# Performance work log

Measured on AMD Instinct MI355X. Metric: run time of the kernel, lower is better.

Reference implementation:

```python
import jax, jax.numpy as jnp
import numpy as np

IN_C = 16
OUT_C = 16
GRID = 8
K = 3  # spline order
RANGE = (-1.0, 1.0)
COEF_M = GRID + K                       # number of B-spline coefficients per (in,out)
SIZE = IN_C * OUT_C * COEF_M + 2 * IN_C * OUT_C  # 3328: coef + univariate_w + residual_w


def _grid():
    # extended knot grid: grid_size intervals over RANGE, padded by K on each side
    h = (RANGE[1] - RANGE[0]) / GRID
    return (np.arange(-K, GRID + K + 1) * h + RANGE[0]).astype(np.float32)


def b_splines(x, grid):
    # x: (N, in) -> bases: (N, in, GRID + K) via Cox-de Boor recursion
    xg = x[..., None]
    bases = ((xg >= grid[:-1]) & (xg < grid[1:])).astype(x.dtype)
    for p in range(1, K + 1):
        left = (xg - grid[:-(p + 1)]) / (grid[p:-1] - grid[:-(p + 1)])
        right = (grid[p + 1:] - xg) / (grid[p + 1:] - grid[1:-p])
        bases = left * bases[..., :-1] + right * bases[..., 1:]
    return bases


def setup_inputs() -> dict:
    key = jax.random.key(0)
    k1, k2 = jax.random.split(key)
    x = jax.random.normal(k1, (2, IN_C, 128, 128), jnp.float32)
    w = jax.random.normal(k2, (2, SIZE, 128, 128), jnp.float32) * 0.1
    return {"x": x, "w": w}


def reference(x, w):
    B, C, H, W = x.shape
    N = B * H * W
    # per-pixel dynamic KAN parameters
    wt = jnp.transpose(w, (0, 2, 3, 1)).reshape(N, SIZE)
    xt = jnp.transpose(x, (0, 2, 3, 1)).reshape(N, IN_C)
    i0 = IN_C * OUT_C * COEF_M
    i1 = i0 + IN_C * OUT_C
    coef = wt[:, :i0].reshape(N, IN_C, OUT_C, COEF_M)
    uw = wt[:, i0:i1].reshape(N, IN_C, OUT_C)
    rw = wt[:, i1:].reshape(N, IN_C, OUT_C)
    grid = jnp.asarray(_grid())
    bases = b_splines(xt, grid)                    # (N, in, M)
    spline = jnp.einsum('niom,nim->nio', coef, bases)  # per-token spline values
    y = jnp.einsum('nio,nio->no', uw, spline) + jnp.einsum('nio,ni->no', rw, jax.nn.silu(xt))
    return jnp.transpose(y.reshape(B, H, W, OUT_C), (0, 3, 1, 2))
```

## Files before the change

### kernel.cpp

```cpp
#include <hip/hip_runtime.h>

#define IN_C   16
#define OUT_C  16
#define COEF_M 11
#define PLANE  16384
#define WSIZE  3328
#define I0     2816
#define I1     3072

__global__ __launch_bounds__(256) void kan_kernel(
    const float* __restrict__ x, const float* __restrict__ w,
    float* __restrict__ out)
{
    const int tid = threadIdx.x;
    const int px  = tid & 63;
    const int g   = tid >> 6;
    const int pixel = blockIdx.x * 64 + px;
    const int b  = pixel >> 14;
    const int hw = pixel & (PLANE - 1);

    const float* wb = w + (size_t)b * WSIZE * PLANE + hw;
    const float* xb = x + (size_t)b * IN_C * PLANE + hw;

    float acc[OUT_C];
    #pragma unroll
    for (int o = 0; o < OUT_C; ++o) acc[o] = 0.0f;

    for (int ii = 0; ii < 4; ++ii) {
        const int i = g * 4 + ii;
        const float xi = xb[(size_t)i * PLANE];

        float bp[14];
        #pragma unroll
        for (int j = 0; j < 14; ++j) {
            const float tj  = -1.75f + 0.25f * j;
            const float tj1 = tj + 0.25f;
            bp[j] = (xi >= tj && xi < tj1) ? 1.0f : 0.0f;
        }
        #pragma unroll
        for (int p = 1; p <= 3; ++p) {
            const float inv = 1.0f / (0.25f * (float)p);
            #pragma unroll
            for (int j = 0; j < 14 - p; ++j) {
                const float tj    = -1.75f + 0.25f * j;
                const float left  = (xi - tj) * inv;
                const float right = ((tj + 0.25f * (float)(p + 1)) - xi) * inv;
                bp[j] = left * bp[j] + right * bp[j + 1];
            }
        }

        const float sx = xi / (1.0f + __expf(-xi));

        const float* ci = wb + (size_t)(i * (OUT_C * COEF_M)) * PLANE;
        const float* ui = wb + (size_t)(I0 + i * OUT_C) * PLANE;
        const float* ri = wb + (size_t)(I1 + i * OUT_C) * PLANE;

        #pragma unroll
        for (int o = 0; o < OUT_C; ++o) {
            const float* c = ci + (size_t)(o * COEF_M) * PLANE;
            float sp = 0.0f;
            #pragma unroll
            for (int m = 0; m < COEF_M; ++m)
                sp += c[(size_t)m * PLANE] * bp[m];
            acc[o] += ui[(size_t)o * PLANE] * sp + ri[(size_t)o * PLANE] * sx;
        }
    }

    __shared__ float red[4 * 64 * 17];
    #pragma unroll
    for (int o = 0; o < OUT_C; ++o)
        red[(g * 64 + px) * 17 + o] = acc[o];
    __syncthreads();

    const int og = g;
    #pragma unroll
    for (int k = 0; k < 4; ++k) {
        const int o = og * 4 + k;
        const float s = red[(0 * 64 + px) * 17 + o]
                      + red[(1 * 64 + px) * 17 + o]
                      + red[(2 * 64 + px) * 17 + o]
                      + red[(3 * 64 + px) * 17 + o];
        out[(size_t)b * (OUT_C * PLANE) + (size_t)o * PLANE + hw] = s;
    }
}

extern "C" void kernel_launch(void* const* d_in, const int* in_sizes, int n_in,
                              void* d_out, int out_size, void* d_ws, size_t ws_size,
                              hipStream_t stream) {
    const float* x = (const float*)d_in[0];
    const float* w = (const float*)d_in[1];
    float* out = (float*)d_out;

    kan_kernel<<<dim3(512), dim3(256), 0, stream>>>(x, w, out);
}
```

Before: 560.3 us.

## Vectorize pixel loads to float4 and split output channels across blocks

```diff
diff --git a/kernel.cpp b/kernel.cpp
--- a/kernel.cpp
+++ b/kernel.cpp
@@ -3,85 +3,102 @@
 #define IN_C   16
 #define OUT_C  16
 #define COEF_M 11
-#define PLANE  16384
+#define PLANE4 4096
 #define WSIZE  3328
 #define I0     2816
 #define I1     3072
 
-__global__ __launch_bounds__(256) void kan_kernel(
+__device__ __forceinline__ float4 f4_mul(float4 a, float4 b) {
+    return make_float4(a.x*b.x, a.y*b.y, a.z*b.z, a.w*b.w);
+}
+__device__ __forceinline__ float4 f4_fma(float4 a, float4 b, float4 c) {
+    return make_float4(fmaf(a.x,b.x,c.x), fmaf(a.y,b.y,c.y),
+                       fmaf(a.z,b.z,c.z), fmaf(a.w,b.w,c.w));
+}
+__device__ __forceinline__ float4 f4_add(float4 a, float4 b) {
+    return make_float4(a.x+b.x, a.y+b.y, a.z+b.z, a.w+b.w);
+}
+
+__global__ __launch_bounds__(256, 2) void kan_kernel(
     const float* __restrict__ x, const float* __restrict__ w,
     float* __restrict__ out)
 {
     const int tid = threadIdx.x;
-    const int px  = tid & 63;
+    const int l   = tid & 63;
     const int g   = tid >> 6;
-    const int pixel = blockIdx.x * 64 + px;
-    const int b  = pixel >> 14;
-    const int hw = pixel & (PLANE - 1);
+    const int pg  = blockIdx.x >> 2;
+    const int oq  = blockIdx.x & 3;
+    const int o_base = oq * 4;
 
-    const float* wb = w + (size_t)b * WSIZE * PLANE + hw;
-    const float* xb = x + (size_t)b * IN_C * PLANE + hw;
+    const int p4 = pg * 64 + l;
+    const int b  = p4 >> 12;
+    const int hw4 = p4 & (PLANE4 - 1);
 
-    float acc[OUT_C];
+    const float4* wb4 = (const float4*)w + (size_t)b * WSIZE * PLANE4 + hw4;
+    const float4* xb4 = (const float4*)x + (size_t)b * IN_C  * PLANE4 + hw4;
+
+    float4 acc[4];
     #pragma unroll
-    for (int o = 0; o < OUT_C; ++o) acc[o] = 0.0f;
+    for (int o = 0; o < 4; ++o) acc[o] = make_float4(0.f, 0.f, 0.f, 0.f);
 
+    #pragma unroll
     for (int ii = 0; ii < 4; ++ii) {
         const int i = g * 4 + ii;
-        const float xi = xb[(size_t)i * PLANE];
+        const float4 xv = xb4[(size_t)i * PLANE4];
 
-        float bp[14];
+        float4 bp[14];
         #pragma unroll
         for (int j = 0; j < 14; ++j) {
             const float tj  = -1.75f + 0.25f * j;
             const float tj1 = tj + 0.25f;
-            bp[j] = (xi >= tj && xi < tj1) ? 1.0f : 0.0f;
+            bp[j] = make_float4(
+                (xv.x >= tj && xv.x < tj1) ? 1.f : 0.f,
+                (xv.y >= tj && xv.y < tj1) ? 1.f : 0.f,
+                (xv.z >= tj && xv.z < tj1) ? 1.f : 0.f,
+                (xv.w >= tj && xv.w < tj1) ? 1.f : 0.f);
         }
         #pragma unroll
         for (int p = 1; p <= 3; ++p) {
             const float inv = 1.0f / (0.25f * (float)p);
             #pragma unroll
             for (int j = 0; j < 14 - p; ++j) {
-                const float tj    = -1.75f + 0.25f * j;
-                const float left  = (xi - tj) * inv;
-                const float right = ((tj + 0.25f * (float)(p + 1)) - xi) * inv;
-                bp[j] = left * bp[j] + right * bp[j + 1];
+                const float tj = -1.75f + 0.25f * j;
+                const float tr = tj + 0.25f * (float)(p + 1);
+                float4 left  = make_float4((xv.x - tj)*inv, (xv.y - tj)*inv,
+                                           (xv.z - tj)*inv, (xv.w - tj)*inv);
+                float4 right = make_float4((tr - xv.x)*inv, (tr - xv.y)*inv,
+                                           (tr - xv.z)*inv, (tr - xv.w)*inv);
+                bp[j] = f4_fma(left, bp[j], f4_mul(right, bp[j + 1]));
             }
         }
 
-        const float sx = xi / (1.0f + __expf(-xi));
-
-        const float* ci = wb + (size_t)(i * (OUT_C * COEF_M)) * PLANE;
-        const float* ui = wb + (size_t)(I0 + i * OUT_C) * PLANE;
-        const float* ri = wb + (size_t)(I1 + i * OUT_C) * PLANE;
+        const float4 sx = make_float4(
+            xv.x / (1.f + __expf(-xv.x)), xv.y / (1.f + __expf(-xv.y)),
+            xv.z / (1.f + __expf(-xv.z)), xv.w / (1.f + __expf(-xv.w)));
 
         #pragma unroll
-        for (int o = 0; o < OUT_C; ++o) {
-            const float* c = ci + (size_t)(o * COEF_M) * PLANE;
-            float sp = 0.0f;
+        for (int o = 0; o < 4; ++o) {
+            const int og = o_base + o;
+            const float4* c = wb4 + (size_t)(i * (OUT_C * COEF_M) + og * COEF_M) * PLANE4;
+            float4 sp = make_float4(0.f, 0.f, 0.f, 0.f);
             #pragma unroll
             for (int m = 0; m < COEF_M; ++m)
-                sp += c[(size_t)m * PLANE] * bp[m];
-            acc[o] += ui[(size_t)o * PLANE] * sp + ri[(size_t)o * PLANE] * sx;
+                sp = f4_fma(c[(size_t)m * PLANE4], bp[m], sp);
+            const float4 uwv = wb4[(size_t)(I0 + i * OUT_C + og) * PLANE4];
+            const float4 rwv = wb4[(size_t)(I1 + i * OUT_C + og) * PLANE4];
+            acc[o] = f4_fma(uwv, sp, f4_fma(rwv, sx, acc[o]));
         }
     }
 
-    __shared__ float red[4 * 64 * 17];
+    __shared__ float4 red[4][64][5];
     #pragma unroll
-    for (int o = 0; o < OUT_C; ++o)
-        red[(g * 64 + px) * 17 + o] = acc[o];
+    for (int o = 0; o < 4; ++o) red[g][l][o] = acc[o];
     __syncthreads();
 
-    const int og = g;
-    #pragma unroll
-    for (int k = 0; k < 4; ++k) {
-        const int o = og * 4 + k;
-        const float s = red[(0 * 64 + px) * 17 + o]
-                      + red[(1 * 64 + px) * 17 + o]
-                      + red[(2 * 64 + px) * 17 + o]
-                      + red[(3 * 64 + px) * 17 + o];
-        out[(size_t)b * (OUT_C * PLANE) + (size_t)o * PLANE + hw] = s;
-    }
+    float4 s = f4_add(f4_add(red[0][l][g], red[1][l][g]),
+                      f4_add(red[2][l][g], red[3][l][g]));
+    float4* out4 = (float4*)out;
+    out4[(size_t)b * (OUT_C * PLANE4) + (size_t)(o_base + g) * PLANE4 + hw4] = s;
 }
 
 extern "C" void kernel_launch(void* const* d_in, const int* in_sizes, int n_in,
```

New measurement: 562.9 us. No clear change (+0.5%).

## Vectorize pixels into float4 loads and split output channels across blocks

Applied to the files above, without the earlier changes.

```diff
diff --git a/kernel.cpp b/kernel.cpp
--- a/kernel.cpp
+++ b/kernel.cpp
@@ -3,84 +3,97 @@
 #define IN_C   16
 #define OUT_C  16
 #define COEF_M 11
-#define PLANE  16384
+#define PLANE4 4096
 #define WSIZE  3328
 #define I0     2816
 #define I1     3072
 
-__global__ __launch_bounds__(256) void kan_kernel(
+typedef float f4 __attribute__((ext_vector_type(4)));
+
+__device__ __forceinline__ f4 ldnt(const f4* p) {
+    return __builtin_nontemporal_load(p);
+}
+
+__global__ __launch_bounds__(256, 3) void kan_kernel(
     const float* __restrict__ x, const float* __restrict__ w,
     float* __restrict__ out)
 {
     const int tid = threadIdx.x;
-    const int px  = tid & 63;
+    const int l   = tid & 63;
     const int g   = tid >> 6;
-    const int pixel = blockIdx.x * 64 + px;
-    const int b  = pixel >> 14;
-    const int hw = pixel & (PLANE - 1);
+    const int pg  = blockIdx.x >> 3;
+    const int oq  = blockIdx.x & 7;
+    const int o0  = oq * 2;
 
-    const float* wb = w + (size_t)b * WSIZE * PLANE + hw;
-    const float* xb = x + (size_t)b * IN_C * PLANE + hw;
+    const int p4  = pg * 64 + l;
+    const int b   = p4 >> 12;
+    const int hw4 = p4 & (PLANE4 - 1);
 
-    float acc[OUT_C];
+    const f4* wb4 = (const f4*)w + (size_t)b * WSIZE * PLANE4 + hw4;
+    const f4* xb4 = (const f4*)x + (size_t)b * IN_C  * PLANE4 + hw4;
+
+    f4 acc[2];
+    acc[0] = f4{0.f, 0.f, 0.f, 0.f};
+    acc[1] = f4{0.f, 0.f, 0.f, 0.f};
+
     #pragma unroll
-    for (int o = 0; o < OUT_C; ++o) acc[o] = 0.0f;
-
     for (int ii = 0; ii < 4; ++ii) {
         const int i = g * 4 + ii;
-        const float xi = xb[(size_t)i * PLANE];
+        const f4 xv = xb4[(size_t)i * PLANE4];
 
-        float bp[14];
+        f4 bp[14];
         #pragma unroll
         for (int j = 0; j < 14; ++j) {
             const float tj  = -1.75f + 0.25f * j;
             const float tj1 = tj + 0.25f;
-            bp[j] = (xi >= tj && xi < tj1) ? 1.0f : 0.0f;
+            f4 v;
+            v.x = (xv.x >= tj && xv.x < tj1) ? 1.f : 0.f;
+            v.y = (xv.y >= tj && xv.y < tj1) ? 1.f : 0.f;
+            v.z = (xv.z >= tj && xv.z < tj1) ? 1.f : 0.f;
+            v.w = (xv.w >= tj && xv.w < tj1) ? 1.f : 0.f;
+            bp[j] = v;
         }
         #pragma unroll
         for (int p = 1; p <= 3; ++p) {
-            const float inv = 1.0f / (0.25f * (float)p);
+            const float inv = 4.0f / (float)p;
             #pragma unroll
             for (int j = 0; j < 14 - p; ++j) {
-                const float tj    = -1.75f + 0.25f * j;
-                const float left  = (xi - tj) * inv;
-                const float right = ((tj + 0.25f * (float)(p + 1)) - xi) * inv;
-                bp[j] = left * bp[j] + right * bp[j + 1];
+                const float tj = -1.75f + 0.25f * j;
+                const float tr = tj + 0.25f * (float)(p + 1);
+                bp[j] = ((xv - tj) * inv) * bp[j] + ((tr - xv) * inv) * bp[j + 1];
             }
         }
 
-        const float sx = xi / (1.0f + __expf(-xi));
-
-        const float* ci = wb + (size_t)(i * (OUT_C * COEF_M)) * PLANE;
-        const float* ui = wb + (size_t)(I0 + i * OUT_C) * PLANE;
-        const float* ri = wb + (size_t)(I1 + i * OUT_C) * PLANE;
+        f4 sx;
+        sx.x = xv.x / (1.f + __expf(-xv.x));
+        sx.y = xv.y / (1.f + __expf(-xv.y));
+        sx.z = xv.z / (1.f + __expf(-xv.z));
+        sx.w = xv.w / (1.f + __expf(-xv.w));
 
         #pragma unroll
-        for (int o = 0; o < OUT_C; ++o) {
-            const float* c = ci + (size_t)(o * COEF_M) * PLANE;
-            float sp = 0.0f;
+        for (int oo = 0; oo < 2; ++oo) {
+            const int o = o0 + oo;
+            const f4* c = wb4 + (size_t)(i * (OUT_C * COEF_M) + o * COEF_M) * PLANE4;
+            f4 sp = f4{0.f, 0.f, 0.f, 0.f};
             #pragma unroll
             for (int m = 0; m < COEF_M; ++m)
-                sp += c[(size_t)m * PLANE] * bp[m];
-            acc[o] += ui[(size_t)o * PLANE] * sp + ri[(size_t)o * PLANE] * sx;
+                sp += ldnt(c + (size_t)m * PLANE4) * bp[m];
+            const f4 uwv = ldnt(wb4 + (size_t)(I0 + i * OUT_C + o) * PLANE4);
+            const f4 rwv = ldnt(wb4 + (size_t)(I1 + i * OUT_C + o) * PLANE4);
+            acc[oo] += uwv * sp + rwv * sx;
         }
     }
 
-    __shared__ float red[4 * 64 * 17];
-    #pragma unroll
-    for (int o = 0; o < OUT_C; ++o)
-        red[(g * 64 + px) * 17 + o] = acc[o];
+    __shared__ f4 red[4][64][3];
+    red[g][l][0] = acc[0];
+    red[g][l][1] = acc[1];
     __syncthreads();
 
-    const int og = g;
-    #pragma unroll
-    for (int k = 0; k < 4; ++k) {
-        const int o = og * 4 + k;
-        const float s = red[(0 * 64 + px) * 17 + o]
-                      + red[(1 * 64 + px) * 17 + o]
-                      + red[(2 * 64 + px) * 17 + o]
-                      + red[(3 * 64 + px) * 17 + o];
-        out[(size_t)b * (OUT_C * PLANE) + (size_t)o * PLANE + hw] = s;
+    if (g < 2) {
+        f4 s = red[0][l][g] + red[1][l][g] + red[2][l][g] + red[3][l][g];
+        f4* out4 = (f4*)out;
+        __builtin_nontemporal_store(
+            s, out4 + (size_t)b * (OUT_C * PLANE4) + (size_t)(o0 + g) * PLANE4 + hw4);
     }
 }
 
@@ -91,5 +104,5 @@
     const float* w = (const float*)d_in[1];
     float* out = (float*)d_out;
 
-    kan_kernel<<<dim3(512), dim3(256), 0, stream>>>(x, w, out);
+    kan_kernel<<<dim3(1024), dim3(256), 0, stream>>>(x, w, out);
 }
```

Result: slower. 605.1 us (+8.0%).
